# Kernel tuning notes

Measured on AMD Instinct MI355X. Metric: run time of the kernel, lower is better.

Reference implementation:

```python
import jax, jax.numpy as jnp
import numpy as np

WINDOW_SIZE = 11
SIGMA = 1.5
NUM_CHANNEL = 1
C1 = 0.01 ** 2
C2 = 0.03 ** 2


def _gaussian_window(window_size: int, sigma: float, num_channel: int) -> jnp.ndarray:
    x = np.arange(window_size, dtype=np.float32)
    g = np.exp(-((x - window_size // 2) ** 2) / (2.0 * sigma ** 2))
    g = g / g.sum()
    w2d = np.outer(g, g).astype(np.float32)  # [K, K]
    # OIHW depthwise kernel: [C, 1, K, K]
    return jnp.asarray(np.broadcast_to(w2d, (num_channel, 1, window_size, window_size)).copy())


def _dwconv(x: jnp.ndarray, window: jnp.ndarray) -> jnp.ndarray:
    k = window.shape[-1]
    pad = k // 2
    return jax.lax.conv_general_dilated(
        x, window,
        window_strides=(1, 1),
        padding=[(pad, pad), (pad, pad)],
        dimension_numbers=("NCHW", "OIHW", "NCHW"),
        feature_group_count=x.shape[1],
    )


def setup_inputs() -> dict:
    key = jax.random.key(0)
    k1, k2 = jax.random.split(key)
    shape = (32, 1, 512, 512)
    X_gt = jax.random.uniform(k1, shape, dtype=jnp.float32)
    X_pred = jax.random.uniform(k2, shape, dtype=jnp.float32)
    return {"X_gt": X_gt, "X_pred": X_pred}


def reference(X_gt, X_pred):
    window = _gaussian_window(WINDOW_SIZE, SIGMA, X_gt.shape[1]).astype(X_gt.dtype)
    mu1 = _dwconv(X_gt, window)
    mu2 = _dwconv(X_pred, window)
    sq_mu1 = mu1 * mu1
    sq_mu2 = mu2 * mu2
    sigma1 = _dwconv(X_gt * X_gt, window) - sq_mu1
    sigma2 = _dwconv(X_pred * X_pred, window) - sq_mu2
    sigma = _dwconv(X_gt * X_pred, window) - mu1 * mu2
    ssim_map = ((2.0 * (mu1 * mu2) + C1) * (2.0 * sigma + C2)) / (
        (sq_mu1 + sq_mu2 + C1) * (sq_mu1 + sq_mu2 + C2)
    )
    # size_average=True -> scalar mean
    return ssim_map.mean()
```

## Files before the change

### kernel.cpp

```cpp
#include <hip/hip_runtime.h>
#include <math.h>

#define IMG_H 512
#define IMG_W 512
#define KW 11
#define RAD 5
#define T 8
#define NG (IMG_W / 4)

#define C1F (0.01f * 0.01f)
#define C2F (0.03f * 0.03f)

__device__ __forceinline__ float ssim_px(float mu1, float mu2, float sp) {
    float m12 = mu1 * mu2;
    float sigma = sp - m12;
    float sq = mu1 * mu1 + mu2 * mu2;
    return ((2.f * m12 + C1F) * (2.f * sigma + C2F)) / ((sq + C1F) * (sq + C2F));
}

__global__ __launch_bounds__(256, 2)
void ssim_fused_kernel(const float* __restrict__ A, const float* __restrict__ B,
                       float* __restrict__ out, float inv_total) {
    __shared__ float wpart[4];

    const int tid = threadIdx.x;
    const int g = tid & (NG - 1);
    const int rchunk = tid >> 7;
    const int img = blockIdx.y;
    const int ybase = blockIdx.x * (2 * T) + rchunk * T;

    float w[KW];
    {
        float s = 0.f;
#pragma unroll
        for (int i = 0; i < KW; ++i) {
            float d = (float)(i - RAD);
            w[i] = expf(-(d * d) / 4.5f);
            s += w[i];
        }
        float inv = 1.0f / s;
#pragma unroll
        for (int i = 0; i < KW; ++i) {
            w[i] *= inv;
            w[i] = __int_as_float(__builtin_amdgcn_readfirstlane(__float_as_int(w[i])));
        }
    }

    const float* __restrict__ Ai = A + (size_t)img * IMG_H * IMG_W;
    const float* __restrict__ Bi = B + (size_t)img * IMG_H * IMG_W;

    float4 accA[T], accB[T], accP[T];
#pragma unroll
    for (int o = 0; o < T; ++o) {
        accA[o] = make_float4(0.f, 0.f, 0.f, 0.f);
        accB[o] = accA[o];
        accP[o] = accA[o];
    }

#pragma unroll
    for (int i = 0; i < T + 2 * RAD; ++i) {
        int gy = ybase + i - RAD;
        if (gy >= 0 && gy < IMG_H) {
            const float* rowA = Ai + (size_t)gy * IMG_W;
            const float* rowB = Bi + (size_t)gy * IMG_W;

            float fa[20], fb[20];
#pragma unroll
            for (int m = 0; m < 5; ++m) {
                int gm = g + m - 2;
                float4 va = make_float4(0.f, 0.f, 0.f, 0.f);
                float4 vb = va;
                if ((unsigned)gm < (unsigned)NG) {
                    va = *(const float4*)(rowA + 4 * gm);
                    vb = *(const float4*)(rowB + 4 * gm);
                }
                fa[4 * m] = va.x; fa[4 * m + 1] = va.y; fa[4 * m + 2] = va.z; fa[4 * m + 3] = va.w;
                fb[4 * m] = vb.x; fb[4 * m + 1] = vb.y; fb[4 * m + 2] = vb.z; fb[4 * m + 3] = vb.w;
            }

            float4 hA = make_float4(0.f, 0.f, 0.f, 0.f);
            float4 hB = hA, hP = hA;
#pragma unroll
            for (int k = 0; k < KW; ++k) {
                float wk = w[k];
                hA.x += wk * fa[3 + k];  hA.y += wk * fa[4 + k];
                hA.z += wk * fa[5 + k];  hA.w += wk * fa[6 + k];
                hB.x += wk * fb[3 + k];  hB.y += wk * fb[4 + k];
                hB.z += wk * fb[5 + k];  hB.w += wk * fb[6 + k];
                hP.x += wk * (fa[3 + k] * fb[3 + k]);
                hP.y += wk * (fa[4 + k] * fb[4 + k]);
                hP.z += wk * (fa[5 + k] * fb[5 + k]);
                hP.w += wk * (fa[6 + k] * fb[6 + k]);
            }

#pragma unroll
            for (int o = 0; o < T; ++o) {
                if (i - o >= 0 && i - o < KW) {
                    float wk = w[i - o];
                    accA[o].x += wk * hA.x; accA[o].y += wk * hA.y;
                    accA[o].z += wk * hA.z; accA[o].w += wk * hA.w;
                    accB[o].x += wk * hB.x; accB[o].y += wk * hB.y;
                    accB[o].z += wk * hB.z; accB[o].w += wk * hB.w;
                    accP[o].x += wk * hP.x; accP[o].y += wk * hP.y;
                    accP[o].z += wk * hP.z; accP[o].w += wk * hP.w;
                }
            }
        }
    }

    float acc = 0.f;
#pragma unroll
    for (int o = 0; o < T; ++o) {
        acc += ssim_px(accA[o].x, accB[o].x, accP[o].x);
        acc += ssim_px(accA[o].y, accB[o].y, accP[o].y);
        acc += ssim_px(accA[o].z, accB[o].z, accP[o].z);
        acc += ssim_px(accA[o].w, accB[o].w, accP[o].w);
    }

#pragma unroll
    for (int off = 32; off > 0; off >>= 1)
        acc += __shfl_down(acc, off, 64);
    int wid = tid >> 6;
    int lane = tid & 63;
    if (lane == 0) wpart[wid] = acc;
    __syncthreads();
    if (tid == 0) {
        float s = (wpart[0] + wpart[1]) + (wpart[2] + wpart[3]);
        atomicAdd(out, s * inv_total);
    }
}

extern "C" void kernel_launch(void* const* d_in, const int* in_sizes, int n_in,
                              void* d_out, int out_size, void* d_ws, size_t ws_size,
                              hipStream_t stream) {
    const float* A = (const float*)d_in[0];
    const float* B = (const float*)d_in[1];
    float* out = (float*)d_out;

    const int total = in_sizes[0];
    const int nimg = total / (IMG_H * IMG_W);

    hipMemsetAsync(d_out, 0, sizeof(float), stream);

    dim3 grid(IMG_H / (2 * T), nimg, 1);
    ssim_fused_kernel<<<grid, 256, 0, stream>>>(A, B, out, 1.0f / (float)total);
}
```

Measured before the change: 142.3 us.

## Halve rows per thread, roll row loop, and trim horizontal halo loads

Cuts the outputs per thread from 8 rows to 4, which halves the accumulator registers and doubles the number of blocks. The row loop is no longer unrolled, and the vertical weight is fetched by dynamic index from a small shared-memory copy. The horizontal halo now loads three float4s plus two scalar edge elements per row instead of five float4s, and the products are precomputed once per row. In exchange, the halo rows are re-read more often (14 rows read per 4 output rows versus 18 per 8), which adds global and L2 traffic, and the rolled loop adds per-iteration overhead and LDS reads.

```diff
diff --git a/kernel.cpp b/kernel.cpp
--- a/kernel.cpp
+++ b/kernel.cpp
@@ -5,7 +5,8 @@
 #define IMG_W 512
 #define KW 11
 #define RAD 5
-#define T 8
+#define T 4
+#define NROWS (T + 2 * RAD)
 #define NG (IMG_W / 4)
 
 #define C1F (0.01f * 0.01f)
@@ -21,6 +22,7 @@
 __global__ __launch_bounds__(256, 2)
 void ssim_fused_kernel(const float* __restrict__ A, const float* __restrict__ B,
                        float* __restrict__ out, float inv_total) {
+    __shared__ float wlds[KW];
     __shared__ float wpart[4];
 
     const int tid = threadIdx.x;
@@ -45,64 +47,84 @@
             w[i] = __int_as_float(__builtin_amdgcn_readfirstlane(__float_as_int(w[i])));
         }
     }
+    if (tid == 0) {
+        wlds[0] = w[0]; wlds[1] = w[1]; wlds[2]  = w[2];  wlds[3] = w[3];
+        wlds[4] = w[4]; wlds[5] = w[5]; wlds[6]  = w[6];  wlds[7] = w[7];
+        wlds[8] = w[8]; wlds[9] = w[9]; wlds[10] = w[10];
+    }
+    __syncthreads();
 
     const float* __restrict__ Ai = A + (size_t)img * IMG_H * IMG_W;
     const float* __restrict__ Bi = B + (size_t)img * IMG_H * IMG_W;
+    const int c0 = 4 * g;
 
-    float4 accA[T], accB[T], accP[T];
+    float accA[T][4], accB[T][4], accP[T][4];
 #pragma unroll
-    for (int o = 0; o < T; ++o) {
-        accA[o] = make_float4(0.f, 0.f, 0.f, 0.f);
-        accB[o] = accA[o];
-        accP[o] = accA[o];
-    }
+    for (int o = 0; o < T; ++o)
+#pragma unroll
+        for (int c = 0; c < 4; ++c) {
+            accA[o][c] = 0.f; accB[o][c] = 0.f; accP[o][c] = 0.f;
+        }
 
+#pragma unroll 1
+    for (int i = 0; i < NROWS; ++i) {
+        const int gy = ybase + i - RAD;
+        if (gy >= 0 && gy < IMG_H) {
+            const float* rA = Ai + (size_t)gy * IMG_W;
+            const float* rB = Bi + (size_t)gy * IMG_W;
+
+            const float4 z4 = make_float4(0.f, 0.f, 0.f, 0.f);
+            float4 va0 = z4, vb0 = z4, va2 = z4, vb2 = z4;
+            if (g >= 1) {
+                va0 = *(const float4*)(rA + c0 - 4);
+                vb0 = *(const float4*)(rB + c0 - 4);
+            }
+            float4 va1 = *(const float4*)(rA + c0);
+            float4 vb1 = *(const float4*)(rB + c0);
+            if (g <= NG - 2) {
+                va2 = *(const float4*)(rA + c0 + 4);
+                vb2 = *(const float4*)(rB + c0 + 4);
+            }
+            float eaL = 0.f, ebL = 0.f, eaR = 0.f, ebR = 0.f;
+            if (c0 - 5 >= 0)    { eaL = rA[c0 - 5]; ebL = rB[c0 - 5]; }
+            if (c0 + 8 < IMG_W) { eaR = rA[c0 + 8]; ebR = rB[c0 + 8]; }
+
+            float fa[14] = {eaL, va0.x, va0.y, va0.z, va0.w,
+                            va1.x, va1.y, va1.z, va1.w,
+                            va2.x, va2.y, va2.z, va2.w, eaR};
+            float fb[14] = {ebL, vb0.x, vb0.y, vb0.z, vb0.w,
+                            vb1.x, vb1.y, vb1.z, vb1.w,
+                            vb2.x, vb2.y, vb2.z, vb2.w, ebR};
+            float p[14];
 #pragma unroll
-    for (int i = 0; i < T + 2 * RAD; ++i) {
-        int gy = ybase + i - RAD;
-        if (gy >= 0 && gy < IMG_H) {
-            const float* rowA = Ai + (size_t)gy * IMG_W;
-            const float* rowB = Bi + (size_t)gy * IMG_W;
+            for (int j = 0; j < 14; ++j) p[j] = fa[j] * fb[j];
 
-            float fa[20], fb[20];
-#pragma unroll
-            for (int m = 0; m < 5; ++m) {
-                int gm = g + m - 2;
-                float4 va = make_float4(0.f, 0.f, 0.f, 0.f);
-                float4 vb = va;
-                if ((unsigned)gm < (unsigned)NG) {
-                    va = *(const float4*)(rowA + 4 * gm);
-                    vb = *(const float4*)(rowB + 4 * gm);
-                }
-                fa[4 * m] = va.x; fa[4 * m + 1] = va.y; fa[4 * m + 2] = va.z; fa[4 * m + 3] = va.w;
-                fb[4 * m] = vb.x; fb[4 * m + 1] = vb.y; fb[4 * m + 2] = vb.z; fb[4 * m + 3] = vb.w;
-            }
-
-            float4 hA = make_float4(0.f, 0.f, 0.f, 0.f);
-            float4 hB = hA, hP = hA;
+            float hA[4] = {0.f, 0.f, 0.f, 0.f};
+            float hB[4] = {0.f, 0.f, 0.f, 0.f};
+            float hP[4] = {0.f, 0.f, 0.f, 0.f};
 #pragma unroll
             for (int k = 0; k < KW; ++k) {
                 float wk = w[k];
-                hA.x += wk * fa[3 + k];  hA.y += wk * fa[4 + k];
-                hA.z += wk * fa[5 + k];  hA.w += wk * fa[6 + k];
-                hB.x += wk * fb[3 + k];  hB.y += wk * fb[4 + k];
-                hB.z += wk * fb[5 + k];  hB.w += wk * fb[6 + k];
-                hP.x += wk * (fa[3 + k] * fb[3 + k]);
-                hP.y += wk * (fa[4 + k] * fb[4 + k]);
-                hP.z += wk * (fa[5 + k] * fb[5 + k]);
-                hP.w += wk * (fa[6 + k] * fb[6 + k]);
+#pragma unroll
+                for (int c = 0; c < 4; ++c) {
+                    hA[c] += wk * fa[k + c];
+                    hB[c] += wk * fb[k + c];
+                    hP[c] += wk * p[k + c];
+                }
             }
 
 #pragma unroll
             for (int o = 0; o < T; ++o) {
-                if (i - o >= 0 && i - o < KW) {
-                    float wk = w[i - o];
-                    accA[o].x += wk * hA.x; accA[o].y += wk * hA.y;
-                    accA[o].z += wk * hA.z; accA[o].w += wk * hA.w;
-                    accB[o].x += wk * hB.x; accB[o].y += wk * hB.y;
-                    accB[o].z += wk * hB.z; accB[o].w += wk * hB.w;
-                    accP[o].x += wk * hP.x; accP[o].y += wk * hP.y;
-                    accP[o].z += wk * hP.z; accP[o].w += wk * hP.w;
+                int k = i - o;
+                bool v = ((unsigned)k < (unsigned)KW);
+                int kc = v ? k : 0;
+                float wk = wlds[kc];
+                wk = v ? wk : 0.f;
+#pragma unroll
+                for (int c = 0; c < 4; ++c) {
+                    accA[o][c] += wk * hA[c];
+                    accB[o][c] += wk * hB[c];
+                    accP[o][c] += wk * hP[c];
                 }
             }
         }
@@ -110,12 +132,10 @@
 
     float acc = 0.f;
 #pragma unroll
-    for (int o = 0; o < T; ++o) {
-        acc += ssim_px(accA[o].x, accB[o].x, accP[o].x);
-        acc += ssim_px(accA[o].y, accB[o].y, accP[o].y);
-        acc += ssim_px(accA[o].z, accB[o].z, accP[o].z);
-        acc += ssim_px(accA[o].w, accB[o].w, accP[o].w);
-    }
+    for (int o = 0; o < T; ++o)
+#pragma unroll
+        for (int c = 0; c < 4; ++c)
+            acc += ssim_px(accA[o][c], accB[o][c], accP[o][c]);
 
 #pragma unroll
     for (int off = 32; off > 0; off >>= 1)
```

Measured after the change: 163.5 us. 1.15x slower.

## Reorder separable conv: vertical pass in registers, horizontal pass via LDS

Applied to the files above, without the earlier changes.

Restructures the separable Gaussian filter so each thread first does the vertical pass over its own two columns, reading each input row once with coalesced float2 loads. It then writes the vertical results to shared memory and does the horizontal pass from LDS, which removes the redundant overlapping global loads of neighbouring float4 groups. Each block now covers 4 output rows instead of 16, so the 10-row halo is re-read far more often relative to useful rows, and a block barrier plus LDS traffic are added.

```diff
diff --git a/kernel.cpp b/kernel.cpp
--- a/kernel.cpp
+++ b/kernel.cpp
@@ -5,8 +5,9 @@
 #define IMG_W 512
 #define KW 11
 #define RAD 5
-#define T 8
-#define NG (IMG_W / 4)
+#define T 4
+#define NROWS (T + 2 * RAD)
+#define LROW 528
 
 #define C1F (0.01f * 0.01f)
 #define C2F (0.03f * 0.03f)
@@ -21,13 +22,13 @@
 __global__ __launch_bounds__(256, 2)
 void ssim_fused_kernel(const float* __restrict__ A, const float* __restrict__ B,
                        float* __restrict__ out, float inv_total) {
+    __shared__ float sV[3][T][LROW];
     __shared__ float wpart[4];
 
     const int tid = threadIdx.x;
-    const int g = tid & (NG - 1);
-    const int rchunk = tid >> 7;
+    const int c0 = 2 * tid;
     const int img = blockIdx.y;
-    const int ybase = blockIdx.x * (2 * T) + rchunk * T;
+    const int ybase = blockIdx.x * T;
 
     float w[KW];
     {
@@ -46,75 +47,92 @@
         }
     }
 
+    if (tid < 8) {
+#pragma unroll
+        for (int a = 0; a < 3; ++a)
+#pragma unroll
+            for (int r = 0; r < T; ++r) {
+                sV[a][r][tid] = 0.f;
+                sV[a][r][520 + tid] = 0.f;
+            }
+    }
+
     const float* __restrict__ Ai = A + (size_t)img * IMG_H * IMG_W;
     const float* __restrict__ Bi = B + (size_t)img * IMG_H * IMG_W;
 
-    float4 accA[T], accB[T], accP[T];
+    float2 ra[NROWS], rb[NROWS];
+#pragma unroll
+    for (int i = 0; i < NROWS; ++i) {
+        int gy = ybase + i - RAD;
+        float2 a = make_float2(0.f, 0.f);
+        float2 b = make_float2(0.f, 0.f);
+        if (gy >= 0 && gy < IMG_H) {
+            a = *(const float2*)(Ai + (size_t)gy * IMG_W + c0);
+            b = *(const float2*)(Bi + (size_t)gy * IMG_W + c0);
+        }
+        ra[i] = a; rb[i] = b;
+    }
+
+    float2 vA[T], vB[T], vP[T];
 #pragma unroll
     for (int o = 0; o < T; ++o) {
-        accA[o] = make_float4(0.f, 0.f, 0.f, 0.f);
-        accB[o] = accA[o];
-        accP[o] = accA[o];
+        vA[o] = make_float2(0.f, 0.f);
+        vB[o] = make_float2(0.f, 0.f);
+        vP[o] = make_float2(0.f, 0.f);
     }
-
 #pragma unroll
-    for (int i = 0; i < T + 2 * RAD; ++i) {
-        int gy = ybase + i - RAD;
-        if (gy >= 0 && gy < IMG_H) {
-            const float* rowA = Ai + (size_t)gy * IMG_W;
-            const float* rowB = Bi + (size_t)gy * IMG_W;
-
-            float fa[20], fb[20];
+    for (int i = 0; i < NROWS; ++i) {
+        float px = ra[i].x * rb[i].x;
+        float py = ra[i].y * rb[i].y;
 #pragma unroll
-            for (int m = 0; m < 5; ++m) {
-                int gm = g + m - 2;
-                float4 va = make_float4(0.f, 0.f, 0.f, 0.f);
-                float4 vb = va;
-                if ((unsigned)gm < (unsigned)NG) {
-                    va = *(const float4*)(rowA + 4 * gm);
-                    vb = *(const float4*)(rowB + 4 * gm);
-                }
-                fa[4 * m] = va.x; fa[4 * m + 1] = va.y; fa[4 * m + 2] = va.z; fa[4 * m + 3] = va.w;
-                fb[4 * m] = vb.x; fb[4 * m + 1] = vb.y; fb[4 * m + 2] = vb.z; fb[4 * m + 3] = vb.w;
-            }
-
-            float4 hA = make_float4(0.f, 0.f, 0.f, 0.f);
-            float4 hB = hA, hP = hA;
-#pragma unroll
-            for (int k = 0; k < KW; ++k) {
+        for (int o = 0; o < T; ++o) {
+            int k = i - o;
+            if (k >= 0 && k < KW) {
                 float wk = w[k];
-                hA.x += wk * fa[3 + k];  hA.y += wk * fa[4 + k];
-                hA.z += wk * fa[5 + k];  hA.w += wk * fa[6 + k];
-                hB.x += wk * fb[3 + k];  hB.y += wk * fb[4 + k];
-                hB.z += wk * fb[5 + k];  hB.w += wk * fb[6 + k];
-                hP.x += wk * (fa[3 + k] * fb[3 + k]);
-                hP.y += wk * (fa[4 + k] * fb[4 + k]);
-                hP.z += wk * (fa[5 + k] * fb[5 + k]);
-                hP.w += wk * (fa[6 + k] * fb[6 + k]);
-            }
-
-#pragma unroll
-            for (int o = 0; o < T; ++o) {
-                if (i - o >= 0 && i - o < KW) {
-                    float wk = w[i - o];
-                    accA[o].x += wk * hA.x; accA[o].y += wk * hA.y;
-                    accA[o].z += wk * hA.z; accA[o].w += wk * hA.w;
-                    accB[o].x += wk * hB.x; accB[o].y += wk * hB.y;
-                    accB[o].z += wk * hB.z; accB[o].w += wk * hB.w;
-                    accP[o].x += wk * hP.x; accP[o].y += wk * hP.y;
-                    accP[o].z += wk * hP.z; accP[o].w += wk * hP.w;
-                }
+                vA[o].x += wk * ra[i].x; vA[o].y += wk * ra[i].y;
+                vB[o].x += wk * rb[i].x; vB[o].y += wk * rb[i].y;
+                vP[o].x += wk * px;      vP[o].y += wk * py;
             }
         }
     }
 
+#pragma unroll
+    for (int o = 0; o < T; ++o) {
+        *(float2*)&sV[0][o][c0 + 8] = vA[o];
+        *(float2*)&sV[1][o][c0 + 8] = vB[o];
+        *(float2*)&sV[2][o][c0 + 8] = vP[o];
+    }
+    __syncthreads();
+
     float acc = 0.f;
 #pragma unroll
-    for (int o = 0; o < T; ++o) {
-        acc += ssim_px(accA[o].x, accB[o].x, accP[o].x);
-        acc += ssim_px(accA[o].y, accB[o].y, accP[o].y);
-        acc += ssim_px(accA[o].z, accB[o].z, accP[o].z);
-        acc += ssim_px(accA[o].w, accB[o].w, accP[o].w);
+    for (int r = 0; r < T; ++r) {
+        float2 qa[7], qb[7], qp[7];
+#pragma unroll
+        for (int j = 0; j < 7; ++j) {
+            qa[j] = *(const float2*)&sV[0][r][c0 + 2 + 2 * j];
+            qb[j] = *(const float2*)&sV[1][r][c0 + 2 + 2 * j];
+            qp[j] = *(const float2*)&sV[2][r][c0 + 2 + 2 * j];
+        }
+        float fa[14] = {qa[0].x, qa[0].y, qa[1].x, qa[1].y, qa[2].x, qa[2].y,
+                        qa[3].x, qa[3].y, qa[4].x, qa[4].y, qa[5].x, qa[5].y,
+                        qa[6].x, qa[6].y};
+        float fb[14] = {qb[0].x, qb[0].y, qb[1].x, qb[1].y, qb[2].x, qb[2].y,
+                        qb[3].x, qb[3].y, qb[4].x, qb[4].y, qb[5].x, qb[5].y,
+                        qb[6].x, qb[6].y};
+        float fp[14] = {qp[0].x, qp[0].y, qp[1].x, qp[1].y, qp[2].x, qp[2].y,
+                        qp[3].x, qp[3].y, qp[4].x, qp[4].y, qp[5].x, qp[5].y,
+                        qp[6].x, qp[6].y};
+        float h0A = 0.f, h1A = 0.f, h0B = 0.f, h1B = 0.f, h0P = 0.f, h1P = 0.f;
+#pragma unroll
+        for (int k = 0; k < KW; ++k) {
+            float wk = w[k];
+            h0A += wk * fa[k + 1]; h1A += wk * fa[k + 2];
+            h0B += wk * fb[k + 1]; h1B += wk * fb[k + 2];
+            h0P += wk * fp[k + 1]; h1P += wk * fp[k + 2];
+        }
+        acc += ssim_px(h0A, h0B, h0P);
+        acc += ssim_px(h1A, h1B, h1P);
     }
 
 #pragma unroll
@@ -142,6 +160,6 @@
 
     hipMemsetAsync(d_out, 0, sizeof(float), stream);
 
-    dim3 grid(IMG_H / (2 * T), nimg, 1);
+    dim3 grid(IMG_H / T, nimg, 1);
     ssim_fused_kernel<<<grid, 256, 0, stream>>>(A, B, out, 1.0f / (float)total);
 }
```

After: 145.5 us. +2.3%, slower.
